# Kernel optimization log

Measured on AMD Instinct MI355X. Metric: run time of the kernel, lower is better.

Reference implementation:

```python
import jax, jax.numpy as jnp
import numpy as np

B, T, D = 4, 2048, 1024
H, DH = 16, 64
GH = H * DH  # == D here
SCALE = DH ** -0.5
LN_EPS = 1e-5


def setup_inputs() -> dict:
    key = jax.random.key(0)
    ks = jax.random.split(key, 8)
    x = jax.random.normal(ks[0], (B, T, D), dtype=jnp.float32)
    attn_mask = jax.random.uniform(ks[1], (T, T), dtype=jnp.float32)
    # LayerNorm params
    gamma = jnp.ones((D,), jnp.float32)
    beta = jnp.zeros((D,), jnp.float32)
    # projection weights, stored (in, out) so y = x @ W
    Wq = jax.random.normal(ks[2], (D, GH), jnp.float32) * (D ** -0.5)
    Wk = jax.random.normal(ks[3], (D, GH), jnp.float32) * (D ** -0.5)
    Wv = jax.random.normal(ks[4], (D, GH), jnp.float32) * (D ** -0.5)
    Wo = jax.random.normal(ks[5], (GH, D), jnp.float32) * (GH ** -0.5)
    bo = jnp.zeros((D,), jnp.float32)
    return {"x": x, "attn_mask": attn_mask, "gamma": gamma, "beta": beta,
            "Wq": Wq, "Wk": Wk, "Wv": Wv, "Wo": Wo, "bo": bo}


def reference(x, attn_mask, gamma, beta, Wq, Wk, Wv, Wo, bo):
    # LayerNorm over last dim
    mu = jnp.mean(x, axis=-1, keepdims=True)
    var = jnp.mean((x - mu) ** 2, axis=-1, keepdims=True)
    xn = (x - mu) * jax.lax.rsqrt(var + LN_EPS) * gamma + beta
    # QKV projections (bias=False), reshape to [B, H, T, DH]
    split = lambda y: y.reshape(B, T, H, DH).transpose(0, 2, 1, 3)
    q = split(xn @ Wq)
    k = split(xn @ Wk)
    v = split(xn @ Wv)
    # scores scaled then MULTIPLICATIVELY masked (post-scale)
    scores = jnp.einsum('bhqd,bhkd->bhqk', q, k) * SCALE
    scores = scores * attn_mask  # broadcast [T,T] over [B,H,T,T]
    probs = jax.nn.softmax(scores, axis=-1)  # dropout p=0 -> identity
    av = jnp.einsum('bhqk,bhkd->bhqd', probs, v)
    av = av.transpose(0, 2, 1, 3).reshape(B, T, GH)
    return av @ Wo + bo
```

## Files before the change

kernel.cpp:

```cpp
#include <hip/hip_runtime.h>

typedef unsigned short u16;
typedef unsigned int u32;
typedef __bf16 bf16x8 __attribute__((ext_vector_type(8)));
typedef float f32x4 __attribute__((ext_vector_type(4)));

#define AS1 __attribute__((address_space(1)))
#define AS3 __attribute__((address_space(3)))

#define SWZB(x) ((x) ^ ((((x) >> 7) & 7) << 4))

__device__ __forceinline__ float bf2f(u16 u) {
    union { u32 i; float f; } v; v.i = ((u32)u) << 16; return v.f;
}
__device__ __forceinline__ u16 f2bf(float f) {
    union { float f; u32 i; } v; v.f = f;
    u32 i = v.i;
    u32 r = (i + 0x7fffu + ((i >> 16) & 1u)) >> 16;
    return (u16)r;
}
__device__ __forceinline__ u32 cvtpk_bf16(float lo, float hi) {
    u32 r;
    asm("v_cvt_pk_bf16_f32 %0, %1, %2" : "=v"(r) : "v"(lo), "v"(hi));
    return r;
}
__device__ __forceinline__ float fexp2(float x) {
    float r;
    asm("v_exp_f32 %0, %1" : "=v"(r) : "v"(x));
    return r;
}
__device__ __forceinline__ void gload_lds16(const u16* src, u16* dst) {
    __builtin_amdgcn_global_load_lds((const AS1 void*)src, (AS3 void*)dst, 16, 0, 0);
}

__global__ __launch_bounds__(256) void transpose1024(const float* __restrict__ in,
                                                     u16* __restrict__ out,
                                                     float scale) {
    __shared__ u16 t[64][65];
    int c = threadIdx.x & 63, r0 = threadIdx.x >> 6;
    int ib = blockIdx.y * 64, jb = blockIdx.x * 64;
    #pragma unroll
    for (int r = r0; r < 64; r += 4)
        t[r][c] = f2bf(in[(size_t)(ib + r) * 1024 + jb + c] * scale);
    __syncthreads();
    #pragma unroll
    for (int r = r0; r < 64; r += 4) out[(size_t)(jb + r) * 1024 + ib + c] = t[c][r];
}

__global__ __launch_bounds__(256) void ln_kernel(const float* __restrict__ x,
                                                 const float* __restrict__ g,
                                                 const float* __restrict__ bb,
                                                 u16* __restrict__ xn) {
    int row = blockIdx.x;
    int tid = threadIdx.x;
    const float* xr = x + (size_t)row * 1024;
    float4 v = *(const float4*)&xr[tid * 4];
    float f0 = v.x, f1 = v.y, f2 = v.z, f3 = v.w;
    float s = f0 + f1 + f2 + f3;
    float sq = f0 * f0 + f1 * f1 + f2 * f2 + f3 * f3;
    #pragma unroll
    for (int m = 1; m < 64; m <<= 1) { s += __shfl_xor(s, m, 64); sq += __shfl_xor(sq, m, 64); }
    __shared__ float red[8];
    int wid = tid >> 6, lane = tid & 63;
    if (lane == 0) { red[wid] = s; red[4 + wid] = sq; }
    __syncthreads();
    s = red[0] + red[1] + red[2] + red[3];
    sq = red[4] + red[5] + red[6] + red[7];
    float mu = s * (1.f / 1024.f);
    float var = sq * (1.f / 1024.f) - mu * mu;
    float rs = rsqrtf(var + 1e-5f);
    float4 gv = *(const float4*)&g[tid * 4];
    float4 bv = *(const float4*)&bb[tid * 4];
    ushort4 o;
    o.x = f2bf((f0 - mu) * rs * gv.x + bv.x);
    o.y = f2bf((f1 - mu) * rs * gv.y + bv.y);
    o.z = f2bf((f2 - mu) * rs * gv.z + bv.z);
    o.w = f2bf((f3 - mu) * rs * gv.w + bv.w);
    *(ushort4*)&xn[(size_t)row * 1024 + tid * 4] = o;
}

__global__ __launch_bounds__(256) void gemm_bt(const u16* __restrict__ A,
                                               const u16* __restrict__ BT,
                                               u16* __restrict__ C16,
                                               float* __restrict__ C32,
                                               const float* __restrict__ bias,
                                               int K, int ldc, int ext,
                                               u16* __restrict__ vTout) {
    __shared__ __align__(16) u16 lA[128 * 32];
    __shared__ __align__(16) u16 lB[128 * 32];
    int tid = threadIdx.x, lane = tid & 63, wid = tid >> 6;
    int wr = wid >> 1, wc = wid & 1;
    int m0 = blockIdx.y * 128, n0 = blockIdx.x * 128;
    int l4 = lane >> 4, l15 = lane & 15;

    f32x4 acc[4][4] = {};
    int NT = K >> 5;

    auto stage = [&](int kt) {
        int k0 = kt << 5;
        #pragma unroll
        for (int i = 0; i < 2; ++i) {
            int j = wid * 2 + i;
            int row = j * 16 + (lane >> 2);
            int ch = (lane & 3) * 8;
            gload_lds16(A + (size_t)(m0 + row) * K + k0 + ch, &lA[j * 512]);
            gload_lds16(BT + (size_t)(n0 + row) * K + k0 + ch, &lB[j * 512]);
        }
    };
    stage(0);
    for (int kt = 0; kt < NT; ++kt) {
        __syncthreads();
        bf16x8 af[4], bfr[4];
        #pragma unroll
        for (int i = 0; i < 4; ++i) {
            af[i]  = *(const bf16x8*)&lA[(wr * 64 + i * 16 + l15) * 32 + l4 * 8];
            bfr[i] = *(const bf16x8*)&lB[(wc * 64 + i * 16 + l15) * 32 + l4 * 8];
        }
        __syncthreads();
        if (kt + 1 < NT) stage(kt + 1);
        #pragma unroll
        for (int i = 0; i < 4; ++i)
            #pragma unroll
            for (int j = 0; j < 4; ++j)
                acc[i][j] = __builtin_amdgcn_mfma_f32_16x16x32_bf16(af[i], bfr[j], acc[i][j], 0, 0, 0);
    }
    bool vblk = (vTout != nullptr) && (n0 >= 2048);
    #pragma unroll
    for (int j = 0; j < 4; ++j) {
        int col = n0 + wc * 64 + j * 16 + l15;
        if (vblk) {
            int hd = col - 2048;
            #pragma unroll
            for (int i = 0; i < 4; ++i) {
                int trow = m0 + wr * 64 + i * 16 + l4 * 4;
                int bidx = trow >> 11, t = trow & 2047;
                ushort4 pk;
                pk.x = f2bf(acc[i][j][0]);
                pk.y = f2bf(acc[i][j][1]);
                pk.z = f2bf(acc[i][j][2]);
                pk.w = f2bf(acc[i][j][3]);
                *(ushort4*)&vTout[(size_t)(bidx * 1024 + hd) * 2048 + t] = pk;
            }
        } else {
            float bv = ext ? bias[col] : 0.f;
            #pragma unroll
            for (int i = 0; i < 4; ++i) {
                #pragma unroll
                for (int r = 0; r < 4; ++r) {
                    int row = m0 + wr * 64 + i * 16 + l4 * 4 + r;
                    float val = acc[i][j][r] + bv;
                    if (ext) C32[(size_t)row * ldc + col] = val;
                    else     C16[(size_t)row * ldc + col] = f2bf(val);
                }
            }
        }
    }
}

__global__ __launch_bounds__(256) void attn_kernel(const u16* __restrict__ qkv,
                                                   const u16* __restrict__ vT,
                                                   const float* __restrict__ mask,
                                                   u16* __restrict__ av) {
    __shared__ __align__(16) u16 lK[2][64 * 64];
    __shared__ __align__(16) u16 lV[2][64 * 64];
    int qt = blockIdx.x, bh = blockIdx.y;
    int b = bh >> 4, h = bh & 15;
    int tid = threadIdx.x, lane = tid & 63, wid = tid >> 6;
    int l4 = lane >> 4, l15 = lane & 15;
    int qw = qt * 128 + wid * 32;

    const u16* qb0 = qkv + (size_t)(b * 2048 + qw + l15) * 3072 + h * 64;
    const u16* qb1 = qb0 + (size_t)16 * 3072;
    bf16x8 qf00 = *(const bf16x8*)&qb0[l4 * 8];
    bf16x8 qf01 = *(const bf16x8*)&qb0[32 + l4 * 8];
    bf16x8 qf10 = *(const bf16x8*)&qb1[l4 * 8];
    bf16x8 qf11 = *(const bf16x8*)&qb1[32 + l4 * 8];
    const float* mrow0 = mask + (size_t)(qw + l15) * 2048 + 8 * l4;
    const float* mrow1 = mrow0 + (size_t)16 * 2048;

    f32x4 o0[4] = {}, o1[4] = {};
    float lsum0 = 0.f, lsum1 = 0.f;

    int c0 = tid, c1 = 256 + tid;
    auto pmap = [](int g) {
        return (g & 32) + 4 * ((g >> 3) & 3) + (g & 3) + ((g & 4) << 2);
    };
    int kd0 = SWZB(pmap(c0 >> 3) * 128 + (c0 & 7) * 16);
    int kd1 = SWZB(pmap(c1 >> 3) * 128 + (c1 & 7) * 16);
    int vd0 = SWZB((c0 >> 3) * 128 + (c0 & 7) * 16);
    int vd1 = SWZB((c1 >> 3) * 128 + (c1 & 7) * 16);
    const u16* ksrc0 = qkv + (size_t)(b * 2048 + (c0 >> 3)) * 3072 + 1024 + h * 64 + (c0 & 7) * 8;
    const u16* ksrc1 = qkv + (size_t)(b * 2048 + (c1 >> 3)) * 3072 + 1024 + h * 64 + (c1 & 7) * 8;
    const u16* vsrc0 = vT + (size_t)(bh * 64 + (c0 >> 3)) * 2048 + (c0 & 7) * 8;
    const u16* vsrc1 = vT + (size_t)(bh * 64 + (c1 >> 3)) * 2048 + (c1 & 7) * 8;

    auto loadKV = [&](int t, bf16x8& K0, bf16x8& K1, bf16x8& V0, bf16x8& V1) {
        size_t ko = (size_t)t * (64 * 3072);
        int vo = t * 64;
        K0 = *(const bf16x8*)(ksrc0 + ko);
        K1 = *(const bf16x8*)(ksrc1 + ko);
        V0 = *(const bf16x8*)(vsrc0 + vo);
        V1 = *(const bf16x8*)(vsrc1 + vo);
    };

    union PU { u32 u[4]; bf16x8 v; };

    auto body = [&](int t, int pbuf,
                    bf16x8& nK0, bf16x8& nK1, bf16x8& nV0, bf16x8& nV1,
                    bf16x8& fK0, bf16x8& fK1, bf16x8& fV0, bf16x8& fV1) {
        int k0 = t * 64;
        f32x4 mm0[4], mm1[4];
        mm0[0] = *(const f32x4*)(mrow0 + k0);
        mm0[1] = *(const f32x4*)(mrow0 + k0 + 4);
        mm0[2] = *(const f32x4*)(mrow0 + k0 + 32);
        mm0[3] = *(const f32x4*)(mrow0 + k0 + 36);
        mm1[0] = *(const f32x4*)(mrow1 + k0);
        mm1[1] = *(const f32x4*)(mrow1 + k0 + 4);
        mm1[2] = *(const f32x4*)(mrow1 + k0 + 32);
        mm1[3] = *(const f32x4*)(mrow1 + k0 + 36);
        const char* Kb = (const char*)lK[pbuf];
        f32x4 s0[4] = {}, s1[4] = {};
        __builtin_amdgcn_s_setprio(1);
        #pragma unroll
        for (int fj = 0; fj < 4; ++fj) {
            bf16x8 kf0 = *(const bf16x8*)(Kb + SWZB((fj * 16 + l15) * 128 + l4 * 16));
            bf16x8 kf1 = *(const bf16x8*)(Kb + SWZB((fj * 16 + l15) * 128 + 64 + l4 * 16));
            s0[fj] = __builtin_amdgcn_mfma_f32_16x16x32_bf16(kf0, qf00, s0[fj], 0, 0, 0);
            s0[fj] = __builtin_amdgcn_mfma_f32_16x16x32_bf16(kf1, qf01, s0[fj], 0, 0, 0);
            s1[fj] = __builtin_amdgcn_mfma_f32_16x16x32_bf16(kf0, qf10, s1[fj], 0, 0, 0);
            s1[fj] = __builtin_amdgcn_mfma_f32_16x16x32_bf16(kf1, qf11, s1[fj], 0, 0, 0);
        }
        __builtin_amdgcn_s_setprio(0);
        PU pa0[2], pa1[2];
        #pragma unroll
        for (int fj = 0; fj < 4; ++fj) {
            float p0 = fexp2(s0[fj][0] * mm0[fj][0]);
            float p1 = fexp2(s0[fj][1] * mm0[fj][1]);
            float p2 = fexp2(s0[fj][2] * mm0[fj][2]);
            float p3 = fexp2(s0[fj][3] * mm0[fj][3]);
            lsum0 += (p0 + p1) + (p2 + p3);
            int ks = fj >> 1, hf = (fj & 1) * 2;
            pa0[ks].u[hf]     = cvtpk_bf16(p0, p1);
            pa0[ks].u[hf + 1] = cvtpk_bf16(p2, p3);
        }
        #pragma unroll
        for (int fj = 0; fj < 4; ++fj) {
            float p0 = fexp2(s1[fj][0] * mm1[fj][0]);
            float p1 = fexp2(s1[fj][1] * mm1[fj][1]);
            float p2 = fexp2(s1[fj][2] * mm1[fj][2]);
            float p3 = fexp2(s1[fj][3] * mm1[fj][3]);
            lsum1 += (p0 + p1) + (p2 + p3);
            int ks = fj >> 1, hf = (fj & 1) * 2;
            pa1[ks].u[hf]     = cvtpk_bf16(p0, p1);
            pa1[ks].u[hf + 1] = cvtpk_bf16(p2, p3);
        }
        if (t + 1 < 32) {
            char* Kn = (char*)lK[pbuf ^ 1];
            char* Vn = (char*)lV[pbuf ^ 1];
            *(bf16x8*)(Kn + kd0) = nK0;
            *(bf16x8*)(Kn + kd1) = nK1;
            *(bf16x8*)(Vn + vd0) = nV0;
            *(bf16x8*)(Vn + vd1) = nV1;
        }
        if (t + 2 < 32) loadKV(t + 2, fK0, fK1, fV0, fV1);
        const char* Vb = (const char*)lV[pbuf];
        __builtin_amdgcn_s_setprio(1);
        #pragma unroll
        for (int ks = 0; ks < 2; ++ks) {
            #pragma unroll
            for (int fj = 0; fj < 4; ++fj) {
                bf16x8 vf = *(const bf16x8*)(Vb + SWZB((fj * 16 + l15) * 128 + ks * 64 + l4 * 16));
                o0[fj] = __builtin_amdgcn_mfma_f32_16x16x32_bf16(pa0[ks].v, vf, o0[fj], 0, 0, 0);
                o1[fj] = __builtin_amdgcn_mfma_f32_16x16x32_bf16(pa1[ks].v, vf, o1[fj], 0, 0, 0);
            }
        }
        __builtin_amdgcn_s_setprio(0);
        __syncthreads();
    };

    bf16x8 ka0, ka1, va0, va1, kb0, kb1, vb0, vb1;
    loadKV(0, ka0, ka1, va0, va1);
    *(bf16x8*)((char*)lK[0] + kd0) = ka0;
    *(bf16x8*)((char*)lK[0] + kd1) = ka1;
    *(bf16x8*)((char*)lV[0] + vd0) = va0;
    *(bf16x8*)((char*)lV[0] + vd1) = va1;
    loadKV(1, kb0, kb1, vb0, vb1);
    __syncthreads();
    for (int t = 0; t < 32; t += 2) {
        body(t,     0, kb0, kb1, vb0, vb1, ka0, ka1, va0, va1);
        body(t + 1, 1, ka0, ka1, va0, va1, kb0, kb1, vb0, vb1);
    }

    lsum0 += __shfl_xor(lsum0, 16, 64);
    lsum0 += __shfl_xor(lsum0, 32, 64);
    lsum1 += __shfl_xor(lsum1, 16, 64);
    lsum1 += __shfl_xor(lsum1, 32, 64);
    float den0[4], den1[4];
    #pragma unroll
    for (int r = 0; r < 4; ++r) {
        den0[r] = __shfl(lsum0, l4 * 4 + r, 64);
        den1[r] = __shfl(lsum1, l4 * 4 + r, 64);
    }
    #pragma unroll
    for (int fj = 0; fj < 4; ++fj) {
        #pragma unroll
        for (int r = 0; r < 4; ++r) {
            int col = h * 64 + fj * 16 + l15;
            av[(size_t)(b * 2048 + qw + l4 * 4 + r) * 1024 + col]      = f2bf(o0[fj][r] / den0[r]);
            av[(size_t)(b * 2048 + qw + 16 + l4 * 4 + r) * 1024 + col] = f2bf(o1[fj][r] / den1[r]);
        }
    }
}

extern "C" void kernel_launch(void* const* d_in, const int* in_sizes, int n_in,
                              void* d_out, int out_size, void* d_ws, size_t ws_size,
                              hipStream_t stream) {
    (void)in_sizes; (void)n_in; (void)out_size; (void)ws_size;
    const float* x     = (const float*)d_in[0];
    const float* mask  = (const float*)d_in[1];
    const float* gamma = (const float*)d_in[2];
    const float* beta  = (const float*)d_in[3];
    const float* Wq    = (const float*)d_in[4];
    const float* Wk    = (const float*)d_in[5];
    const float* Wv    = (const float*)d_in[6];
    const float* Wo    = (const float*)d_in[7];
    const float* bo    = (const float*)d_in[8];

    char* ws = (char*)d_ws;
    u16* xn   = (u16*)(ws);
    u16* WT   = (u16*)(ws + 16777216);
    u16* WoT  = (u16*)(ws + 16777216 + 6291456);
    u16* qkvb = (u16*)(ws + 16777216 + 6291456 + 2097152);
    u16* vT   = (u16*)(ws + 16777216 + 6291456 + 2097152 + 50331648);
    u16* av = xn;

    dim3 tb(256);
    transpose1024<<<dim3(16, 16), tb, 0, stream>>>(Wq, WT, 0.18033688f);
    transpose1024<<<dim3(16, 16), tb, 0, stream>>>(Wk, WT + 1024 * 1024, 1.0f);
    transpose1024<<<dim3(16, 16), tb, 0, stream>>>(Wv, WT + 2 * 1024 * 1024, 1.0f);
    transpose1024<<<dim3(16, 16), tb, 0, stream>>>(Wo, WoT, 1.0f);
    ln_kernel<<<8192, tb, 0, stream>>>(x, gamma, beta, xn);
    gemm_bt<<<dim3(24, 64), tb, 0, stream>>>(xn, WT, qkvb, nullptr, nullptr, 1024, 3072, 0, vT);
    attn_kernel<<<dim3(16, 64), tb, 0, stream>>>(qkvb, vT, mask, av);
    gemm_bt<<<dim3(8, 64), tb, 0, stream>>>(av, WoT, nullptr, (float*)d_out, bo, 1024, 1024, 1, nullptr);
}
```

Measured before the change: 267.4 us.

## Merge weight transposes into one launch and remap GEMM blocks per XCD

The four weight transpose launches become a single launch that uses blockIdx.z to pick the matrix, cutting three kernel launches. The GEMM now uses a 1D grid and remaps block IDs so that each of the 8 XCDs owns a contiguous range of N-tile columns. The aim is better L2 reuse of the B (weight) tiles within each XCD. The remap assumes nbx is divisible by 8, which holds for 24 and 8.

```diff
diff --git a/kernel.cpp b/kernel.cpp
--- a/kernel.cpp
+++ b/kernel.cpp
@@ -33,10 +33,17 @@
     __builtin_amdgcn_global_load_lds((const AS1 void*)src, (AS3 void*)dst, 16, 0, 0);
 }
 
-__global__ __launch_bounds__(256) void transpose1024(const float* __restrict__ in,
-                                                     u16* __restrict__ out,
-                                                     float scale) {
+__global__ __launch_bounds__(256) void transposeW(const float* __restrict__ Wq,
+                                                  const float* __restrict__ Wk,
+                                                  const float* __restrict__ Wv,
+                                                  const float* __restrict__ Wo,
+                                                  u16* __restrict__ WT,
+                                                  u16* __restrict__ WoT) {
     __shared__ u16 t[64][65];
+    int z = blockIdx.z;
+    const float* in = (z == 0) ? Wq : (z == 1) ? Wk : (z == 2) ? Wv : Wo;
+    u16* out = (z < 3) ? WT + (size_t)z * 1024 * 1024 : WoT;
+    float scale = (z == 0) ? 0.18033688f : 1.0f;
     int c = threadIdx.x & 63, r0 = threadIdx.x >> 6;
     int ib = blockIdx.y * 64, jb = blockIdx.x * 64;
     #pragma unroll
@@ -84,13 +91,17 @@
                                                u16* __restrict__ C16,
                                                float* __restrict__ C32,
                                                const float* __restrict__ bias,
-                                               int K, int ldc, int ext,
+                                               int K, int ldc, int ext, int nbx,
                                                u16* __restrict__ vTout) {
     __shared__ __align__(16) u16 lA[128 * 32];
     __shared__ __align__(16) u16 lB[128 * 32];
+    int bid = blockIdx.x;
+    int xcd = bid & 7, loc = bid >> 3;
+    int npx = nbx >> 3;
+    int n0 = (xcd * npx + loc % npx) * 128;
+    int m0 = (loc / npx) * 128;
     int tid = threadIdx.x, lane = tid & 63, wid = tid >> 6;
     int wr = wid >> 1, wc = wid & 1;
-    int m0 = blockIdx.y * 128, n0 = blockIdx.x * 128;
     int l4 = lane >> 4, l15 = lane & 15;
 
     f32x4 acc[4][4] = {};
@@ -335,12 +346,9 @@
     u16* av = xn;
 
     dim3 tb(256);
-    transpose1024<<<dim3(16, 16), tb, 0, stream>>>(Wq, WT, 0.18033688f);
-    transpose1024<<<dim3(16, 16), tb, 0, stream>>>(Wk, WT + 1024 * 1024, 1.0f);
-    transpose1024<<<dim3(16, 16), tb, 0, stream>>>(Wv, WT + 2 * 1024 * 1024, 1.0f);
-    transpose1024<<<dim3(16, 16), tb, 0, stream>>>(Wo, WoT, 1.0f);
+    transposeW<<<dim3(16, 16, 4), tb, 0, stream>>>(Wq, Wk, Wv, Wo, WT, WoT);
     ln_kernel<<<8192, tb, 0, stream>>>(x, gamma, beta, xn);
-    gemm_bt<<<dim3(24, 64), tb, 0, stream>>>(xn, WT, qkvb, nullptr, nullptr, 1024, 3072, 0, vT);
+    gemm_bt<<<24 * 64, tb, 0, stream>>>(xn, WT, qkvb, nullptr, nullptr, 1024, 3072, 0, 24, vT);
     attn_kernel<<<dim3(16, 64), tb, 0, stream>>>(qkvb, vT, mask, av);
-    gemm_bt<<<dim3(8, 64), tb, 0, stream>>>(av, WoT, nullptr, (float*)d_out, bo, 1024, 1024, 1, nullptr);
-}
+    gemm_bt<<<8 * 64, tb, 0, stream>>>(av, WoT, nullptr, (float*)d_out, bo, 1024, 1024, 1, 8, nullptr);
+}
```

New measurement: 259.7 us. -2.9%, faster.
